# Optimization experiments

Measured on AMD Instinct MI355X. Metric: run time of the kernel, lower is better.

The kernel has to match this reference:

```python
import jax, jax.numpy as jnp
import numpy as np

Z_DIM, HID, DENSE, OUT = 4096, 1024, 100, 100
B, W = 8, 512


def setup_inputs() -> dict:
    key = jax.random.key(0)
    ks = jax.random.split(key, 16)

    def lin_w(k, fan_in, shape):
        return (jax.random.normal(k, shape, jnp.float32) / np.sqrt(fan_in)).astype(jnp.float32)

    return {
        "z": jax.random.normal(ks[0], (B, W, Z_DIM), jnp.float32),
        "noise": jax.random.uniform(ks[1], (B, W, OUT), jnp.float32),  # torch.rand_like -> U[0,1)
        # LGSSM linear: z_dim -> z_dim (stored as (in, out))
        "W_lgssm": lin_w(ks[2], Z_DIM, (Z_DIM, Z_DIM)),
        "b_lgssm": jnp.zeros((Z_DIM,), jnp.float32),
        # GRU (1 layer): gates ordered [r, z, n] as in torch, stored (in, 3H)
        "W_ih": lin_w(ks[3], Z_DIM, (Z_DIM, 3 * HID)),
        "b_ih": jnp.zeros((3 * HID,), jnp.float32),
        "W_hh": lin_w(ks[4], HID, (HID, 3 * HID)),
        "b_hh": jnp.zeros((3 * HID,), jnp.float32),
        # dense: hidden -> dense
        "W_dense": lin_w(ks[5], HID, (HID, DENSE)),
        "b_dense": jnp.zeros((DENSE,), jnp.float32),
        # mu / sigma heads: dense -> out
        "W_mu": lin_w(ks[6], DENSE, (DENSE, OUT)),
        "b_mu": jnp.zeros((OUT,), jnp.float32),
        "W_sigma": lin_w(ks[7], DENSE, (DENSE, OUT)),
        "b_sigma": jnp.zeros((OUT,), jnp.float32),
    }


def reference(z, noise, W_lgssm, b_lgssm, W_ih, b_ih, W_hh, b_hh,
              W_dense, b_dense, W_mu, b_mu, W_sigma, b_sigma):
    # Sequential per-timestep recurrence: LGSSM linear -> 1-step GRU -> dense
    # -> (mu, softplus(sigma)) -> reparameterized sample mu + sigma * eps.
    def step(h, xs):
        x_t, eps_t = xs                         # (B, Z_DIM), (B, OUT)
        x = x_t @ W_lgssm + b_lgssm             # LGSSM linear
        gi = x @ W_ih + b_ih                    # (B, 3H)
        gh = h @ W_hh + b_hh                    # (B, 3H)
        i_r, i_u, i_n = jnp.split(gi, 3, axis=-1)
        h_r, h_u, h_n = jnp.split(gh, 3, axis=-1)
        r = jax.nn.sigmoid(i_r + h_r)
        u = jax.nn.sigmoid(i_u + h_u)
        n = jnp.tanh(i_n + r * h_n)
        h_new = (1.0 - u) * n + u * h           # torch GRU update
        d = h_new @ W_dense + b_dense
        mu = d @ W_mu + b_mu
        sigma = jax.nn.softplus(d @ W_sigma + b_sigma)
        return h_new, mu + sigma * eps_t

    h0 = jnp.zeros((z.shape[0], W_hh.shape[0]), z.dtype)
    _, outs = jax.lax.scan(step, h0, (jnp.swapaxes(z, 0, 1), jnp.swapaxes(noise, 0, 1)))
    return jnp.swapaxes(outs, 0, 1)             # (B, W, OUT)
```

## Files before the change

### kernel.cpp

```cpp
#include <hip/hip_runtime.h>
#include <cmath>

#define ZD    4096
#define HID   1024
#define G3    3072
#define DN    100
#define OD    100
#define BB    8
#define WW    512
#define ROWS  4096

__device__ __forceinline__ void store_dc(float* p, float v) {
    __hip_atomic_store(p, v, __ATOMIC_RELAXED, __HIP_MEMORY_SCOPE_AGENT);
}

__device__ __forceinline__ unsigned short f2bf(float x) {
    unsigned u = __float_as_uint(x);
    u += 0x7FFFu + ((u >> 16) & 1u);
    return (unsigned short)(u >> 16);
}
__device__ __forceinline__ float bf2f(unsigned short h) {
    return __uint_as_float(((unsigned)h) << 16);
}

typedef short          s16x8 __attribute__((ext_vector_type(8)));
typedef unsigned short u16x8 __attribute__((ext_vector_type(8)));
typedef float          f32x4 __attribute__((ext_vector_type(4)));

__global__ __launch_bounds__(256) void split_T(
    const float* __restrict__ S, unsigned short* __restrict__ Th,
    unsigned short* __restrict__ Tl, int K, int N)
{
    __shared__ float ts[32][33];
    const int tx = threadIdx.x & 31;
    const int ty = threadIdx.x >> 5;
    const int n0 = blockIdx.x << 5;
    const int k0 = blockIdx.y << 5;
    #pragma unroll
    for (int i = 0; i < 4; ++i)
        ts[ty + (i << 3)][tx] = S[(size_t)(k0 + ty + (i << 3)) * N + n0 + tx];
    __syncthreads();
    #pragma unroll
    for (int i = 0; i < 4; ++i) {
        const int nrow = ty + (i << 3);
        const float v = ts[tx][nrow];
        const unsigned short h = f2bf(v);
        const size_t o = (size_t)(n0 + nrow) * K + k0 + tx;
        Th[o] = h;
        Tl[o] = f2bf(v - bf2f(h));
    }
}

#define LP 56

__global__ __launch_bounds__(256) void gemm_bf16x3_ws(
    const float* __restrict__ A,
    const unsigned short* __restrict__ BTh,
    const unsigned short* __restrict__ BTl,
    const float* __restrict__ bias,
    unsigned short* __restrict__ Ch,
    unsigned short* __restrict__ Cl,
    int M, int N, int K)
{
    __shared__ __align__(16) unsigned short Ah[128][LP];
    __shared__ __align__(16) unsigned short Al[128][LP];
    __shared__ __align__(16) unsigned short Bh[128][LP];
    __shared__ __align__(16) unsigned short Bl[128][LP];

    const int tid  = threadIdx.x;
    const int lane = tid & 63;
    const int wid  = tid >> 6;
    const int wm   = (wid >> 1) << 6;
    const int wn   = (wid & 1) << 6;
    const int l16  = lane & 15;
    const int gq   = lane >> 4;
    const int bn0  = blockIdx.x << 7;
    const int bm0  = blockIdx.y << 7;

    f32x4 acc[4][4];
    #pragma unroll
    for (int i = 0; i < 4; ++i)
        #pragma unroll
        for (int j = 0; j < 4; ++j)
            acc[i][j] = (f32x4){0.f, 0.f, 0.f, 0.f};

    const int r0 = tid >> 2;
    const int c8 = (tid & 3) << 3;

    for (int k0 = 0; k0 < K; k0 += 32) {
        __syncthreads();
        #pragma unroll
        for (int it = 0; it < 2; ++it) {
            const int r = r0 + (it << 6);
            const float* ap = A + (size_t)(bm0 + r) * K + k0 + c8;
            const float4 f0 = *(const float4*)ap;
            const float4 f1 = *(const float4*)(ap + 4);
            const float fv[8] = {f0.x, f0.y, f0.z, f0.w, f1.x, f1.y, f1.z, f1.w};
            u16x8 vh, vl;
            #pragma unroll
            for (int j = 0; j < 8; ++j) {
                const unsigned short h = f2bf(fv[j]);
                vh[j] = h;
                vl[j] = f2bf(fv[j] - bf2f(h));
            }
            *(u16x8*)&Ah[r][c8] = vh;
            *(u16x8*)&Al[r][c8] = vl;
            const size_t boff = (size_t)(bn0 + r) * K + k0 + c8;
            *(u16x8*)&Bh[r][c8] = *(const u16x8*)(BTh + boff);
            *(u16x8*)&Bl[r][c8] = *(const u16x8*)(BTl + boff);
        }
        __syncthreads();

        s16x8 afh[4], afl[4];
        #pragma unroll
        for (int mi = 0; mi < 4; ++mi) {
            afh[mi] = *(const s16x8*)&Ah[wm + (mi << 4) + l16][gq << 3];
            afl[mi] = *(const s16x8*)&Al[wm + (mi << 4) + l16][gq << 3];
        }
        #pragma unroll
        for (int ni = 0; ni < 4; ++ni) {
            const s16x8 bfh = *(const s16x8*)&Bh[wn + (ni << 4) + l16][gq << 3];
            const s16x8 bfl = *(const s16x8*)&Bl[wn + (ni << 4) + l16][gq << 3];
            #pragma unroll
            for (int mi = 0; mi < 4; ++mi) {
                acc[mi][ni] = __builtin_amdgcn_mfma_f32_16x16x32_bf16(afh[mi], bfh, acc[mi][ni], 0, 0, 0);
                acc[mi][ni] = __builtin_amdgcn_mfma_f32_16x16x32_bf16(afh[mi], bfl, acc[mi][ni], 0, 0, 0);
                acc[mi][ni] = __builtin_amdgcn_mfma_f32_16x16x32_bf16(afl[mi], bfh, acc[mi][ni], 0, 0, 0);
            }
        }
    }

    #pragma unroll
    for (int ni = 0; ni < 4; ++ni) {
        const int col = bn0 + wn + (ni << 4) + l16;
        const float bv = bias[col];
        #pragma unroll
        for (int mi = 0; mi < 4; ++mi) {
            const int rowb = bm0 + wm + (mi << 4) + (gq << 2);
            #pragma unroll
            for (int r = 0; r < 4; ++r) {
                const float v = acc[mi][ni][r] + bv;
                const size_t o = (size_t)(rowb + r) * N + col;
                const unsigned short h = f2bf(v);
                Ch[o] = h;
                Cl[o] = f2bf(v - bf2f(h));
            }
        }
    }
}

__global__ __launch_bounds__(256) void gemm_bf16x3_pre(
    const unsigned short* __restrict__ ATh,
    const unsigned short* __restrict__ ATl,
    const unsigned short* __restrict__ BTh,
    const unsigned short* __restrict__ BTl,
    const float* __restrict__ bias,
    float* __restrict__ C,
    int M, int N, int K)
{
    __shared__ __align__(16) unsigned short Ah[128][LP];
    __shared__ __align__(16) unsigned short Al[128][LP];
    __shared__ __align__(16) unsigned short Bh[128][LP];
    __shared__ __align__(16) unsigned short Bl[128][LP];

    const int tid  = threadIdx.x;
    const int lane = tid & 63;
    const int wid  = tid >> 6;
    const int wm   = (wid >> 1) << 6;
    const int wn   = (wid & 1) << 6;
    const int l16  = lane & 15;
    const int gq   = lane >> 4;
    const int bn0  = blockIdx.x << 7;
    const int bm0  = blockIdx.y << 7;

    f32x4 acc[4][4];
    #pragma unroll
    for (int i = 0; i < 4; ++i)
        #pragma unroll
        for (int j = 0; j < 4; ++j)
            acc[i][j] = (f32x4){0.f, 0.f, 0.f, 0.f};

    const int r0 = tid >> 2;
    const int c8 = (tid & 3) << 3;

    for (int k0 = 0; k0 < K; k0 += 32) {
        __syncthreads();
        #pragma unroll
        for (int it = 0; it < 2; ++it) {
            const int r = r0 + (it << 6);
            const size_t aoff = (size_t)(bm0 + r) * K + k0 + c8;
            const size_t boff = (size_t)(bn0 + r) * K + k0 + c8;
            *(u16x8*)&Ah[r][c8] = *(const u16x8*)(ATh + aoff);
            *(u16x8*)&Al[r][c8] = *(const u16x8*)(ATl + aoff);
            *(u16x8*)&Bh[r][c8] = *(const u16x8*)(BTh + boff);
            *(u16x8*)&Bl[r][c8] = *(const u16x8*)(BTl + boff);
        }
        __syncthreads();

        s16x8 afh[4], afl[4];
        #pragma unroll
        for (int mi = 0; mi < 4; ++mi) {
            afh[mi] = *(const s16x8*)&Ah[wm + (mi << 4) + l16][gq << 3];
            afl[mi] = *(const s16x8*)&Al[wm + (mi << 4) + l16][gq << 3];
        }
        #pragma unroll
        for (int ni = 0; ni < 4; ++ni) {
            const s16x8 bfh = *(const s16x8*)&Bh[wn + (ni << 4) + l16][gq << 3];
            const s16x8 bfl = *(const s16x8*)&Bl[wn + (ni << 4) + l16][gq << 3];
            #pragma unroll
            for (int mi = 0; mi < 4; ++mi) {
                acc[mi][ni] = __builtin_amdgcn_mfma_f32_16x16x32_bf16(afh[mi], bfh, acc[mi][ni], 0, 0, 0);
                acc[mi][ni] = __builtin_amdgcn_mfma_f32_16x16x32_bf16(afh[mi], bfl, acc[mi][ni], 0, 0, 0);
                acc[mi][ni] = __builtin_amdgcn_mfma_f32_16x16x32_bf16(afl[mi], bfh, acc[mi][ni], 0, 0, 0);
            }
        }
    }

    #pragma unroll
    for (int ni = 0; ni < 4; ++ni) {
        const int col = bn0 + wn + (ni << 4) + l16;
        const float bv = bias[col];
        #pragma unroll
        for (int mi = 0; mi < 4; ++mi) {
            const int rowb = bm0 + wm + (mi << 4) + (gq << 2);
            float* cp = C + (size_t)rowb * N + col;
            #pragma unroll
            for (int r = 0; r < 4; ++r)
                cp[(size_t)r * N] = acc[mi][ni][r] + bv;
        }
    }
}

#define BM 64
#define BN 128
#define BK 16

__global__ __launch_bounds__(256) void gemm_f32(
    const float* __restrict__ A, const float* __restrict__ B,
    const float* __restrict__ bias, float* __restrict__ C,
    int M, int N, int K)
{
    __shared__ __align__(16) float As[BK][BM + 4];
    __shared__ __align__(16) float Bs[BK][BN + 4];
    const int tid = threadIdx.x;
    const int tx = tid & 15;
    const int ty = tid >> 4;
    const int bm0 = blockIdx.y * BM;
    const int bn0 = blockIdx.x * BN;

    float acc[4][8] = {};

    for (int k0 = 0; k0 < K; k0 += BK) {
        {
            const int mr = tid >> 2;
            const int kc = (tid & 3) << 2;
            float4 av = *(const float4*)(A + (size_t)(bm0 + mr) * K + k0 + kc);
            As[kc + 0][mr] = av.x;
            As[kc + 1][mr] = av.y;
            As[kc + 2][mr] = av.z;
            As[kc + 3][mr] = av.w;
        }
        #pragma unroll
        for (int i = 0; i < 2; ++i) {
            const int v = tid + (i << 8);
            const int kr = v >> 5;
            const int nc = (v & 31) << 2;
            *(float4*)&Bs[kr][nc] =
                *(const float4*)(B + (size_t)(k0 + kr) * N + bn0 + nc);
        }
        __syncthreads();
        #pragma unroll
        for (int kk = 0; kk < BK; ++kk) {
            float4 a  = *(const float4*)&As[kk][tx << 2];
            float4 b0 = *(const float4*)&Bs[kk][ty << 3];
            float4 b1 = *(const float4*)&Bs[kk][(ty << 3) + 4];
            const float av[4] = {a.x, a.y, a.z, a.w};
            const float bv[8] = {b0.x, b0.y, b0.z, b0.w, b1.x, b1.y, b1.z, b1.w};
            #pragma unroll
            for (int i = 0; i < 4; ++i)
                #pragma unroll
                for (int j = 0; j < 8; ++j)
                    acc[i][j] = fmaf(av[i], bv[j], acc[i][j]);
        }
        __syncthreads();
    }

    #pragma unroll
    for (int i = 0; i < 4; ++i) {
        const int row = bm0 + (tx << 2) + i;
        float* crow = C + (size_t)row * N + bn0 + (ty << 3);
        const float* brow = bias + bn0 + (ty << 3);
        float4 o0 = make_float4(acc[i][0] + brow[0], acc[i][1] + brow[1],
                                acc[i][2] + brow[2], acc[i][3] + brow[3]);
        float4 o1 = make_float4(acc[i][4] + brow[4], acc[i][5] + brow[5],
                                acc[i][6] + brow[6], acc[i][7] + brow[7]);
        *(float4*)crow = o0;
        *(float4*)(crow + 4) = o1;
    }
}

__global__ __launch_bounds__(256) void recur_kernel(
    const float* __restrict__ GI, const float* __restrict__ Whh,
    const float* __restrict__ bhh, float* __restrict__ Hm,
    unsigned* __restrict__ bar)
{
    __shared__ __align__(16) float hs[BB][HID];
    const int tid = threadIdx.x;
    const int lane = tid & 63;
    const int wv = tid >> 6;
    const int nh = blockIdx.x * 4 + wv;
    unsigned* rel = bar + 2048 + ((blockIdx.x & 31) << 5);

    float wr0[16], wr1[16], wr2[16];
    #pragma unroll
    for (int j = 0; j < 4; ++j)
        #pragma unroll
        for (int q = 0; q < 4; ++q) {
            const int k = (j << 8) + (lane << 2) + q;
            const float* wrow = Whh + (size_t)k * G3;
            wr0[(j << 2) + q] = wrow[nh];
            wr1[(j << 2) + q] = wrow[HID + nh];
            wr2[(j << 2) + q] = wrow[2 * HID + nh];
        }
    const float bh0 = bhh[nh];
    const float bh1 = bhh[HID + nh];
    const float bh2 = bhh[2 * HID + nh];

    float gi_r = 0.f, gi_u = 0.f, gi_n = 0.f;
    if (lane < 8) {
        const float* gp = GI + ((size_t)lane * WW + 0) * G3;
        gi_r = gp[nh];
        gi_u = gp[HID + nh];
        gi_n = gp[2 * HID + nh];
    }

    for (int t = 0; t < WW; ++t) {
        {
            const float4* hp = (const float4*)(Hm + (size_t)t * (BB * HID));
            float4* hd = (float4*)hs;
            #pragma unroll
            for (int i = 0; i < 8; ++i)
                hd[tid + (i << 8)] = hp[tid + (i << 8)];
        }
        float gn_r = 0.f, gn_u = 0.f, gn_n = 0.f;
        if (lane < 8 && t + 1 < WW) {
            const float* gp = GI + ((size_t)lane * WW + (t + 1)) * G3;
            gn_r = gp[nh];
            gn_u = gp[HID + nh];
            gn_n = gp[2 * HID + nh];
        }
        __syncthreads();

        float s0 = 0.f, s1 = 0.f, s2 = 0.f;
        #pragma unroll
        for (int b = 0; b < BB; ++b) {
            const float4* hb = (const float4*)&hs[b][0];
            float p0 = 0.f, p1 = 0.f, p2 = 0.f;
            #pragma unroll
            for (int j = 0; j < 4; ++j) {
                float4 h4 = hb[(j << 6) + lane];
                const float hv[4] = {h4.x, h4.y, h4.z, h4.w};
                #pragma unroll
                for (int q = 0; q < 4; ++q) {
                    p0 = fmaf(hv[q], wr0[(j << 2) + q], p0);
                    p1 = fmaf(hv[q], wr1[(j << 2) + q], p1);
                    p2 = fmaf(hv[q], wr2[(j << 2) + q], p2);
                }
            }
            #pragma unroll
            for (int m = 32; m >= 1; m >>= 1) {
                p0 += __shfl_xor(p0, m, 64);
                p1 += __shfl_xor(p1, m, 64);
                p2 += __shfl_xor(p2, m, 64);
            }
            if (lane == b) { s0 = p0; s1 = p1; s2 = p2; }
        }
        if (lane < 8) {
            const float hold = hs[lane][nh];
            const float r = 1.f / (1.f + expf(-(gi_r + s0 + bh0)));
            const float u = 1.f / (1.f + expf(-(gi_u + s1 + bh1)));
            const float n = tanhf(gi_n + r * (s2 + bh2));
            const float hnew = (1.f - u) * n + u * hold;
            store_dc(Hm + (size_t)(t + 1) * (BB * HID) + lane * HID + nh, hnew);
        }
        __syncthreads();

        if (t < WW - 1) {
            const unsigned want = (unsigned)(t + 1);
            if (tid == 0)
                __hip_atomic_store(bar + blockIdx.x, want,
                                   __ATOMIC_RELAXED, __HIP_MEMORY_SCOPE_AGENT);
            const unsigned root  = (unsigned)t & 255u;
            const unsigned root2 = (root + 128u) & 255u;
            if ((blockIdx.x == root || blockIdx.x == root2) && wv == 0) {
                for (;;) {
                    unsigned v0 = __hip_atomic_load(bar + lane,       __ATOMIC_RELAXED, __HIP_MEMORY_SCOPE_AGENT);
                    unsigned v1 = __hip_atomic_load(bar + lane + 64,  __ATOMIC_RELAXED, __HIP_MEMORY_SCOPE_AGENT);
                    unsigned v2 = __hip_atomic_load(bar + lane + 128, __ATOMIC_RELAXED, __HIP_MEMORY_SCOPE_AGENT);
                    unsigned v3 = __hip_atomic_load(bar + lane + 192, __ATOMIC_RELAXED, __HIP_MEMORY_SCOPE_AGENT);
                    unsigned mn = min(min(v0, v1), min(v2, v3));
                    if (__all(mn >= want)) break;
                }
                if (lane < 32)
                    __hip_atomic_store(bar + 2048 + (lane << 5), want,
                                       __ATOMIC_RELAXED, __HIP_MEMORY_SCOPE_AGENT);
            } else {
                while (__hip_atomic_load(rel, __ATOMIC_RELAXED,
                                         __HIP_MEMORY_SCOPE_AGENT) < want)
                    __builtin_amdgcn_s_sleep(1);
            }
        }
        gi_r = gn_r; gi_u = gn_u; gi_n = gn_n;
    }
}

__global__ __launch_bounds__(128) void head_kernel(
    const float* __restrict__ Hall, const float* __restrict__ Wd,
    const float* __restrict__ bd, const float* __restrict__ Wmu,
    const float* __restrict__ bmu, const float* __restrict__ Wsg,
    const float* __restrict__ bsg, const float* __restrict__ noise,
    float* __restrict__ out)
{
    const int blk = blockIdx.x;
    const int b = blk >> 7;
    const int t0 = (blk & 127) << 2;
    __shared__ __align__(16) float hsh[4][HID];
    __shared__ float dsh[4][DN];
    const int tid = threadIdx.x;

    #pragma unroll
    for (int rr = 0; rr < 4; ++rr) {
        const float4* hp = (const float4*)(Hall + (size_t)(t0 + rr) * (BB * HID) + (size_t)b * HID);
        ((float4*)hsh[rr])[tid] = hp[tid];
        ((float4*)hsh[rr])[tid + 128] = hp[tid + 128];
    }
    __syncthreads();

    if (tid < DN) {
        float a0 = bd[tid], a1 = bd[tid], a2 = bd[tid], a3 = bd[tid];
        for (int k = 0; k < HID; ++k) {
            const float wv = Wd[k * DN + tid];
            a0 = fmaf(hsh[0][k], wv, a0);
            a1 = fmaf(hsh[1][k], wv, a1);
            a2 = fmaf(hsh[2][k], wv, a2);
            a3 = fmaf(hsh[3][k], wv, a3);
        }
        dsh[0][tid] = a0; dsh[1][tid] = a1; dsh[2][tid] = a2; dsh[3][tid] = a3;
    }
    __syncthreads();

    if (tid < OD) {
        float mu[4], sg[4];
        #pragma unroll
        for (int rr = 0; rr < 4; ++rr) { mu[rr] = bmu[tid]; sg[rr] = bsg[tid]; }
        for (int i = 0; i < DN; ++i) {
            const float wm = Wmu[i * OD + tid];
            const float ws = Wsg[i * OD + tid];
            #pragma unroll
            for (int rr = 0; rr < 4; ++rr) {
                const float dv = dsh[rr][i];
                mu[rr] = fmaf(dv, wm, mu[rr]);
                sg[rr] = fmaf(dv, ws, sg[rr]);
            }
        }
        #pragma unroll
        for (int rr = 0; rr < 4; ++rr) {
            const float s = sg[rr];
            const float sp = (s > 20.f) ? s : log1pf(expf(s));
            const size_t oi = (size_t)b * (WW * OD) + (size_t)(t0 + rr) * OD + tid;
            out[oi] = mu[rr] + sp * noise[oi];
        }
    }
}

extern "C" void kernel_launch(void* const* d_in, const int* in_sizes, int n_in,
                              void* d_out, int out_size, void* d_ws, size_t ws_size,
                              hipStream_t stream)
{
    const float* z     = (const float*)d_in[0];
    const float* noise = (const float*)d_in[1];
    const float* W_L   = (const float*)d_in[2];
    const float* b_L   = (const float*)d_in[3];
    const float* W_ih  = (const float*)d_in[4];
    const float* b_ih  = (const float*)d_in[5];
    const float* W_hh  = (const float*)d_in[6];
    const float* b_hh  = (const float*)d_in[7];
    const float* W_d   = (const float*)d_in[8];
    const float* b_d   = (const float*)d_in[9];
    const float* W_mu  = (const float*)d_in[10];
    const float* b_mu  = (const float*)d_in[11];
    const float* W_sg  = (const float*)d_in[12];
    const float* b_sg  = (const float*)d_in[13];
    float* out = (float*)d_out;

    unsigned short* Xh = (unsigned short*)d_ws;
    unsigned short* Xl = Xh + (size_t)ROWS * ZD;
    float* GIb  = (float*)(Xl + (size_t)ROWS * ZD);
    float* Hm   = GIb + (size_t)ROWS * G3;
    unsigned* bar = (unsigned*)(Hm + (size_t)(WW + 1) * (BB * HID));
    unsigned short* WTh = (unsigned short*)((char*)bar + 16384);
    unsigned short* WTl = WTh + (size_t)ZD * ZD;

    const size_t NEED = (size_t)ROWS * ZD * 4 + (size_t)ROWS * G3 * 4
                      + (size_t)(WW + 1) * (BB * HID) * 4 + 16384
                      + 2 * (size_t)ZD * ZD * 2;

    hipMemsetAsync(Hm, 0, (size_t)(BB * HID) * sizeof(float), stream);
    hipMemsetAsync(bar, 0, 16384, stream);

    if (ws_size >= NEED) {
        split_T<<<dim3(ZD / 32, ZD / 32), 256, 0, stream>>>(W_L, WTh, WTl, ZD, ZD);
        gemm_bf16x3_ws<<<dim3(ZD / 128, ROWS / 128), 256, 0, stream>>>(
            z, WTh, WTl, b_L, Xh, Xl, ROWS, ZD, ZD);
        split_T<<<dim3(G3 / 32, ZD / 32), 256, 0, stream>>>(W_ih, WTh, WTl, ZD, G3);
        gemm_bf16x3_pre<<<dim3(G3 / 128, ROWS / 128), 256, 0, stream>>>(
            Xh, Xl, WTh, WTl, b_ih, GIb, ROWS, G3, ZD);
    } else {
        float* Xf = (float*)d_ws;
        gemm_f32<<<dim3(ZD / BN, ROWS / BM), 256, 0, stream>>>(z, W_L, b_L, Xf, ROWS, ZD, ZD);
        gemm_f32<<<dim3(G3 / BN, ROWS / BM), 256, 0, stream>>>(Xf, W_ih, b_ih, GIb, ROWS, G3, ZD);
    }

    void* args[] = { (void*)&GIb, (void*)&W_hh, (void*)&b_hh, (void*)&Hm, (void*)&bar };
    hipLaunchCooperativeKernel((void*)recur_kernel, dim3(HID / 4), dim3(256), args, 0, stream);

    head_kernel<<<dim3(ROWS / 4), 128, 0, stream>>>(Hm + BB * HID, W_d, b_d, W_mu, b_mu, W_sg, b_sg, noise, out);
}
```

Before: 3.853 ms.

## Prefetch next K-tile into registers and swizzle workgroup order in bf16x3 GEMMs

Both split-bf16 GEMM kernels now issue global loads for the next K slice into registers before running the MFMA work on the current slice, so memory latency overlaps with compute. Workgroup IDs are also remapped with an XCD-style swizzle (stride by eight) so that neighbouring tiles sharing A/B rows land on the same die and get better L2 reuse. This raises register pressure and may lower occupancy.

```diff
diff --git a/kernel.cpp b/kernel.cpp
--- a/kernel.cpp
+++ b/kernel.cpp
@@ -67,6 +67,12 @@
     __shared__ __align__(16) unsigned short Bh[128][LP];
     __shared__ __align__(16) unsigned short Bl[128][LP];
 
+    const int nwg  = gridDim.x * gridDim.y;
+    const int flat = blockIdx.y * gridDim.x + blockIdx.x;
+    const int swz  = (flat & 7) * (nwg >> 3) + (flat >> 3);
+    const int bn0  = (swz % gridDim.x) << 7;
+    const int bm0  = (swz / gridDim.x) << 7;
+
     const int tid  = threadIdx.x;
     const int lane = tid & 63;
     const int wid  = tid >> 6;
@@ -74,8 +80,6 @@
     const int wn   = (wid & 1) << 6;
     const int l16  = lane & 15;
     const int gq   = lane >> 4;
-    const int bn0  = blockIdx.x << 7;
-    const int bm0  = blockIdx.y << 7;
 
     f32x4 acc[4][4];
     #pragma unroll
@@ -87,15 +91,29 @@
     const int r0 = tid >> 2;
     const int c8 = (tid & 3) << 3;
 
-    for (int k0 = 0; k0 < K; k0 += 32) {
-        __syncthreads();
+    float4 pa[2][2];
+    u16x8  pbh[2], pbl[2];
+    auto LOADK = [&](int k0) {
         #pragma unroll
         for (int it = 0; it < 2; ++it) {
             const int r = r0 + (it << 6);
             const float* ap = A + (size_t)(bm0 + r) * K + k0 + c8;
-            const float4 f0 = *(const float4*)ap;
-            const float4 f1 = *(const float4*)(ap + 4);
-            const float fv[8] = {f0.x, f0.y, f0.z, f0.w, f1.x, f1.y, f1.z, f1.w};
+            pa[it][0] = *(const float4*)ap;
+            pa[it][1] = *(const float4*)(ap + 4);
+            const size_t boff = (size_t)(bn0 + r) * K + k0 + c8;
+            pbh[it] = *(const u16x8*)(BTh + boff);
+            pbl[it] = *(const u16x8*)(BTl + boff);
+        }
+    };
+
+    LOADK(0);
+    for (int k0 = 0; k0 < K; k0 += 32) {
+        __syncthreads();
+        #pragma unroll
+        for (int it = 0; it < 2; ++it) {
+            const int r = r0 + (it << 6);
+            const float fv[8] = {pa[it][0].x, pa[it][0].y, pa[it][0].z, pa[it][0].w,
+                                 pa[it][1].x, pa[it][1].y, pa[it][1].z, pa[it][1].w};
             u16x8 vh, vl;
             #pragma unroll
             for (int j = 0; j < 8; ++j) {
@@ -105,10 +123,10 @@
             }
             *(u16x8*)&Ah[r][c8] = vh;
             *(u16x8*)&Al[r][c8] = vl;
-            const size_t boff = (size_t)(bn0 + r) * K + k0 + c8;
-            *(u16x8*)&Bh[r][c8] = *(const u16x8*)(BTh + boff);
-            *(u16x8*)&Bl[r][c8] = *(const u16x8*)(BTl + boff);
-        }
+            *(u16x8*)&Bh[r][c8] = pbh[it];
+            *(u16x8*)&Bl[r][c8] = pbl[it];
+        }
+        if (k0 + 32 < K) LOADK(k0 + 32);
         __syncthreads();
 
         s16x8 afh[4], afl[4];
@@ -163,6 +181,12 @@
     __shared__ __align__(16) unsigned short Bh[128][LP];
     __shared__ __align__(16) unsigned short Bl[128][LP];
 
+    const int nwg  = gridDim.x * gridDim.y;
+    const int flat = blockIdx.y * gridDim.x + blockIdx.x;
+    const int swz  = (flat & 7) * (nwg >> 3) + (flat >> 3);
+    const int bn0  = (swz % gridDim.x) << 7;
+    const int bm0  = (swz / gridDim.x) << 7;
+
     const int tid  = threadIdx.x;
     const int lane = tid & 63;
     const int wid  = tid >> 6;
@@ -170,8 +194,6 @@
     const int wn   = (wid & 1) << 6;
     const int l16  = lane & 15;
     const int gq   = lane >> 4;
-    const int bn0  = blockIdx.x << 7;
-    const int bm0  = blockIdx.y << 7;
 
     f32x4 acc[4][4];
     #pragma unroll
@@ -183,18 +205,32 @@
     const int r0 = tid >> 2;
     const int c8 = (tid & 3) << 3;
 
-    for (int k0 = 0; k0 < K; k0 += 32) {
-        __syncthreads();
+    u16x8 pah[2], pal[2], pbh[2], pbl[2];
+    auto LOADK = [&](int k0) {
         #pragma unroll
         for (int it = 0; it < 2; ++it) {
             const int r = r0 + (it << 6);
             const size_t aoff = (size_t)(bm0 + r) * K + k0 + c8;
             const size_t boff = (size_t)(bn0 + r) * K + k0 + c8;
-            *(u16x8*)&Ah[r][c8] = *(const u16x8*)(ATh + aoff);
-            *(u16x8*)&Al[r][c8] = *(const u16x8*)(ATl + aoff);
-            *(u16x8*)&Bh[r][c8] = *(const u16x8*)(BTh + boff);
-            *(u16x8*)&Bl[r][c8] = *(const u16x8*)(BTl + boff);
-        }
+            pah[it] = *(const u16x8*)(ATh + aoff);
+            pal[it] = *(const u16x8*)(ATl + aoff);
+            pbh[it] = *(const u16x8*)(BTh + boff);
+            pbl[it] = *(const u16x8*)(BTl + boff);
+        }
+    };
+
+    LOADK(0);
+    for (int k0 = 0; k0 < K; k0 += 32) {
+        __syncthreads();
+        #pragma unroll
+        for (int it = 0; it < 2; ++it) {
+            const int r = r0 + (it << 6);
+            *(u16x8*)&Ah[r][c8] = pah[it];
+            *(u16x8*)&Al[r][c8] = pal[it];
+            *(u16x8*)&Bh[r][c8] = pbh[it];
+            *(u16x8*)&Bl[r][c8] = pbl[it];
+        }
+        if (k0 + 32 < K) LOADK(k0 + 32);
         __syncthreads();
 
         s16x8 afh[4], afl[4];
```

Result: no change. 3.871 ms (+0.5%).
